# Performance work log

Measured on AMD Instinct MI355X. Metric: run time of the kernel, lower is better.

The kernel has to match this reference:

```python
import jax, jax.numpy as jnp
import numpy as np

EPS = 1e-8  # torch.nn.functional.cosine_similarity default eps


def setup_inputs() -> dict:
    key = jax.random.key(0)
    k1, k2 = jax.random.split(key)
    P, B, D = 64, 512, 1024
    z_list = jax.random.normal(k1, (P, B, D), dtype=jnp.float32)
    z_avg = jax.random.normal(k2, (B, D), dtype=jnp.float32)  # passed but unused (overwritten in forward)
    return {"z_list": z_list, "z_avg": z_avg}


def reference(z_list, z_avg):
    # z_list: (P, B, D). The original overwrites z_avg with the patch mean.
    P, B, _ = z_list.shape
    z_avg = jnp.mean(z_list, axis=0)  # (B, D)

    # cosine_similarity(z_list[p,i], z_avg[j]) via normalize + batched matmul
    zn = z_list / jnp.maximum(jnp.linalg.norm(z_list, axis=-1, keepdims=True), EPS)
    an = z_avg / jnp.maximum(jnp.linalg.norm(z_avg, axis=-1, keepdims=True), EPS)
    cos_sim = jnp.einsum("pbd,cd->pbc", zn, an) - 1.0  # (P, B, B)

    mask = ~jnp.eye(B, dtype=bool)  # zero out diagonal (i == j)
    z_dissim = jnp.sum(cos_sim * mask[None, :, :])
    count = jnp.sum(mask) * P  # B*(B-1)*P
    return z_dissim / count
```

## Files before the change

### kernel.cpp

```cpp
#include <hip/hip_runtime.h>
#include <math.h>

constexpr int P = 64, B = 512, D = 1024;
constexpr int D4 = D / 4;
constexpr int WAVES = 4;
constexpr int PC = P / WAVES;
constexpr int K3B = 32;
constexpr int BPB = B / K3B;
#define EPS 1e-8f

__device__ inline float wave_reduce_sum(float v) {
#pragma unroll
  for (int off = 1; off < 64; off <<= 1) v += __shfl_xor(v, off);
  return v;
}

__device__ inline float dot4(const float4& a, const float4& b) {
  return a.x * b.x + a.y * b.y + a.z * b.z + a.w * b.w;
}

__global__ __launch_bounds__(256) void k_main(const float* __restrict__ z,
                                              float* __restrict__ an,
                                              float* __restrict__ Uv,
                                              float* __restrict__ diag) {
  const int b = blockIdx.x;
  const int t = threadIdx.x;
  const int w = t >> 6;
  const int lane = t & 63;

  __shared__ float4 lds_zs[WAVES][D4];
  __shared__ float4 lds_uu[WAVES][D4];
  __shared__ float red[2 * WAVES];

  float4 zs[4], uu[4];
#pragma unroll
  for (int k = 0; k < 4; ++k) {
    zs[k] = make_float4(0.f, 0.f, 0.f, 0.f);
    uu[k] = make_float4(0.f, 0.f, 0.f, 0.f);
  }

  const size_t pstride = (size_t)B * D4;
  const float4* base = (const float4*)z + ((size_t)(w * PC) * B + b) * D4;

  float4 cur[4];
#pragma unroll
  for (int k = 0; k < 4; ++k) cur[k] = base[k * 64 + lane];

  for (int pp = 0; pp < PC; ++pp) {
    float4 nxt[4];
    if (pp + 1 < PC) {
      const float4* nb = base + (size_t)(pp + 1) * pstride;
#pragma unroll
      for (int k = 0; k < 4; ++k) nxt[k] = nb[k * 64 + lane];
    } else {
#pragma unroll
      for (int k = 0; k < 4; ++k) nxt[k] = cur[k];
    }

    float ss = 0.f;
#pragma unroll
    for (int k = 0; k < 4; ++k) ss += dot4(cur[k], cur[k]);
    ss = wave_reduce_sum(ss);
    const float wgt = 1.0f / fmaxf(sqrtf(ss), EPS);

#pragma unroll
    for (int k = 0; k < 4; ++k) {
      zs[k].x += cur[k].x; zs[k].y += cur[k].y; zs[k].z += cur[k].z; zs[k].w += cur[k].w;
      uu[k].x += wgt * cur[k].x; uu[k].y += wgt * cur[k].y;
      uu[k].z += wgt * cur[k].z; uu[k].w += wgt * cur[k].w;
    }
#pragma unroll
    for (int k = 0; k < 4; ++k) cur[k] = nxt[k];
  }

#pragma unroll
  for (int k = 0; k < 4; ++k) {
    lds_zs[w][k * 64 + lane] = zs[k];
    lds_uu[w][k * 64 + lane] = uu[k];
  }
  __syncthreads();

  float4 zsum = make_float4(0.f, 0.f, 0.f, 0.f);
  float4 usum = make_float4(0.f, 0.f, 0.f, 0.f);
#pragma unroll
  for (int ww = 0; ww < WAVES; ++ww) {
    float4 a = lds_zs[ww][t];
    float4 u = lds_uu[ww][t];
    zsum.x += a.x; zsum.y += a.y; zsum.z += a.z; zsum.w += a.w;
    usum.x += u.x; usum.y += u.y; usum.z += u.z; usum.w += u.w;
  }

  float ss = dot4(zsum, zsum);
  ss = wave_reduce_sum(ss);
  if (lane == 0) red[w] = ss;
  __syncthreads();
  ss = red[0] + red[1] + red[2] + red[3];

  const float inv = 1.0f / fmaxf(sqrtf(ss), (float)P * EPS);
  float4 a4 = make_float4(zsum.x * inv, zsum.y * inv, zsum.z * inv, zsum.w * inv);

  ((float4*)an)[(size_t)b * D4 + t] = a4;
  ((float4*)Uv)[(size_t)b * D4 + t] = usum;

  float dg = dot4(usum, a4);
  dg = wave_reduce_sum(dg);
  if (lane == 0) red[WAVES + w] = dg;
  __syncthreads();
  if (t == 0) diag[b] = red[WAVES] + red[WAVES + 1] + red[WAVES + 2] + red[WAVES + 3];
}

__global__ __launch_bounds__(256) void k3_colsum(const float* __restrict__ an,
                                                 const float* __restrict__ Uv,
                                                 float* __restrict__ Spart,
                                                 float* __restrict__ Tpart) {
  const int blk = blockIdx.x;
  const int t = threadIdx.x;
  float4 s = make_float4(0.f, 0.f, 0.f, 0.f);
  float4 tt = make_float4(0.f, 0.f, 0.f, 0.f);
#pragma unroll 4
  for (int i = 0; i < BPB; ++i) {
    const size_t b = (size_t)blk * BPB + i;
    float4 a = ((const float4*)an)[b * D4 + t];
    float4 u = ((const float4*)Uv)[b * D4 + t];
    s.x += a.x; s.y += a.y; s.z += a.z; s.w += a.w;
    tt.x += u.x; tt.y += u.y; tt.z += u.z; tt.w += u.w;
  }
  ((float4*)Spart)[(size_t)blk * D4 + t] = s;
  ((float4*)Tpart)[(size_t)blk * D4 + t] = tt;
}

__global__ __launch_bounds__(256) void k4_final(const float* __restrict__ Spart,
                                                const float* __restrict__ Tpart,
                                                const float* __restrict__ diag,
                                                float* __restrict__ out) {
  const int t = threadIdx.x;
  __shared__ float red[4];
  float4 S = make_float4(0.f, 0.f, 0.f, 0.f);
  float4 T = make_float4(0.f, 0.f, 0.f, 0.f);
#pragma unroll 4
  for (int blk = 0; blk < K3B; ++blk) {
    float4 s = ((const float4*)Spart)[(size_t)blk * D4 + t];
    float4 u = ((const float4*)Tpart)[(size_t)blk * D4 + t];
    S.x += s.x; S.y += s.y; S.z += s.z; S.w += s.w;
    T.x += u.x; T.y += u.y; T.z += u.z; T.w += u.w;
  }
  float local = dot4(S, T) - diag[t] - diag[t + 256];
  local = wave_reduce_sum(local);
  const int wid = t >> 6;
  if ((t & 63) == 0) red[wid] = local;
  __syncthreads();
  if (t == 0) {
    const float tot = red[0] + red[1] + red[2] + red[3];
    const float count = 64.0f * 512.0f * 511.0f;
    out[0] = tot / count - 1.0f;
  }
}

extern "C" void kernel_launch(void* const* d_in, const int* in_sizes, int n_in,
                              void* d_out, int out_size, void* d_ws, size_t ws_size,
                              hipStream_t stream) {
  const float* z = (const float*)d_in[0];

  float* ws = (float*)d_ws;
  float* an = ws;
  float* Uv = an + (size_t)B * D;
  float* diag = Uv + (size_t)B * D;
  float* Spart = diag + B;
  float* Tpart = Spart + (size_t)K3B * D;

  k_main<<<B, 256, 0, stream>>>(z, an, Uv, diag);
  k3_colsum<<<K3B, 256, 0, stream>>>(an, Uv, Spart, Tpart);
  k4_final<<<1, 256, 0, stream>>>(Spart, Tpart, diag, (float*)d_out);
}
```

Baseline: 36.11 us.

## Double waves per row block and fuse colsum and final into one atomic tail kernel

The main kernel now runs 8 waves per block, each handling fewer patches, to get more memory parallelism, and it zeroes the atomic accumulators from inside the kernel. The separate column-sum and final-reduction kernels become one tail kernel that atomically accumulates S, T and the diagonal sum, then uses a last-block counter to compute the scalar. This removes one launch and the partial-buffer round trip, at the cost of atomic contention and a threadfence-based last-block pattern. The LDS footprint doubles to 64KB per block, which limits occupancy.

```diff
diff --git a/kernel.cpp b/kernel.cpp
--- a/kernel.cpp
+++ b/kernel.cpp
@@ -3,7 +3,7 @@
 
 constexpr int P = 64, B = 512, D = 1024;
 constexpr int D4 = D / 4;
-constexpr int WAVES = 4;
+constexpr int WAVES = 8;
 constexpr int PC = P / WAVES;
 constexpr int K3B = 32;
 constexpr int BPB = B / K3B;
@@ -19,18 +19,24 @@
   return a.x * b.x + a.y * b.y + a.z * b.z + a.w * b.w;
 }
 
-__global__ __launch_bounds__(256) void k_main(const float* __restrict__ z,
-                                              float* __restrict__ an,
-                                              float* __restrict__ Uv,
-                                              float* __restrict__ diag) {
+__global__ __launch_bounds__(512, 4) void k_main(const float* __restrict__ z,
+                                                 float* __restrict__ an,
+                                                 float* __restrict__ Uv,
+                                                 float* __restrict__ diag,
+                                                 float4* __restrict__ zero4) {
   const int b = blockIdx.x;
   const int t = threadIdx.x;
   const int w = t >> 6;
   const int lane = t & 63;
 
+  if (t == 0) {
+    zero4[b] = make_float4(0.f, 0.f, 0.f, 0.f);
+    if (b == 0) zero4[512] = make_float4(0.f, 0.f, 0.f, 0.f);
+  }
+
   __shared__ float4 lds_zs[WAVES][D4];
   __shared__ float4 lds_uu[WAVES][D4];
-  __shared__ float red[2 * WAVES];
+  __shared__ float red[8];
 
   float4 zs[4], uu[4];
 #pragma unroll
@@ -82,39 +88,44 @@
 
   float4 zsum = make_float4(0.f, 0.f, 0.f, 0.f);
   float4 usum = make_float4(0.f, 0.f, 0.f, 0.f);
-#pragma unroll
-  for (int ww = 0; ww < WAVES; ++ww) {
-    float4 a = lds_zs[ww][t];
-    float4 u = lds_uu[ww][t];
-    zsum.x += a.x; zsum.y += a.y; zsum.z += a.z; zsum.w += a.w;
-    usum.x += u.x; usum.y += u.y; usum.z += u.z; usum.w += u.w;
-  }
-
-  float ss = dot4(zsum, zsum);
-  ss = wave_reduce_sum(ss);
-  if (lane == 0) red[w] = ss;
-  __syncthreads();
-  ss = red[0] + red[1] + red[2] + red[3];
-
-  const float inv = 1.0f / fmaxf(sqrtf(ss), (float)P * EPS);
-  float4 a4 = make_float4(zsum.x * inv, zsum.y * inv, zsum.z * inv, zsum.w * inv);
-
-  ((float4*)an)[(size_t)b * D4 + t] = a4;
-  ((float4*)Uv)[(size_t)b * D4 + t] = usum;
-
-  float dg = dot4(usum, a4);
-  dg = wave_reduce_sum(dg);
-  if (lane == 0) red[WAVES + w] = dg;
-  __syncthreads();
-  if (t == 0) diag[b] = red[WAVES] + red[WAVES + 1] + red[WAVES + 2] + red[WAVES + 3];
-}
-
-__global__ __launch_bounds__(256) void k3_colsum(const float* __restrict__ an,
-                                                 const float* __restrict__ Uv,
-                                                 float* __restrict__ Spart,
-                                                 float* __restrict__ Tpart) {
+  if (t < 256) {
+#pragma unroll
+    for (int ww = 0; ww < WAVES; ++ww) {
+      float4 a = lds_zs[ww][t];
+      float4 u = lds_uu[ww][t];
+      zsum.x += a.x; zsum.y += a.y; zsum.z += a.z; zsum.w += a.w;
+      usum.x += u.x; usum.y += u.y; usum.z += u.z; usum.w += u.w;
+    }
+    float ssq = wave_reduce_sum(dot4(zsum, zsum));
+    if (lane == 0) red[w] = ssq;
+  }
+  __syncthreads();
+  if (t < 256) {
+    const float ss2 = red[0] + red[1] + red[2] + red[3];
+    const float inv = 1.0f / fmaxf(sqrtf(ss2), (float)P * EPS);
+    float4 a4 = make_float4(zsum.x * inv, zsum.y * inv, zsum.z * inv, zsum.w * inv);
+
+    ((float4*)an)[(size_t)b * D4 + t] = a4;
+    ((float4*)Uv)[(size_t)b * D4 + t] = usum;
+
+    float dg = wave_reduce_sum(dot4(usum, a4));
+    if (lane == 0) red[4 + w] = dg;
+  }
+  __syncthreads();
+  if (t == 0) diag[b] = red[4] + red[5] + red[6] + red[7];
+}
+
+__global__ __launch_bounds__(256) void k_tail(const float* __restrict__ an,
+                                              const float* __restrict__ Uv,
+                                              const float* __restrict__ diag,
+                                              float* __restrict__ Sfin,
+                                              float* __restrict__ Tfin,
+                                              float* __restrict__ diagsum,
+                                              int* __restrict__ counter,
+                                              float* __restrict__ out) {
   const int blk = blockIdx.x;
   const int t = threadIdx.x;
+
   float4 s = make_float4(0.f, 0.f, 0.f, 0.f);
   float4 tt = make_float4(0.f, 0.f, 0.f, 0.f);
 #pragma unroll 4
@@ -125,34 +136,49 @@
     s.x += a.x; s.y += a.y; s.z += a.z; s.w += a.w;
     tt.x += u.x; tt.y += u.y; tt.z += u.z; tt.w += u.w;
   }
-  ((float4*)Spart)[(size_t)blk * D4 + t] = s;
-  ((float4*)Tpart)[(size_t)blk * D4 + t] = tt;
-}
-
-__global__ __launch_bounds__(256) void k4_final(const float* __restrict__ Spart,
-                                                const float* __restrict__ Tpart,
-                                                const float* __restrict__ diag,
-                                                float* __restrict__ out) {
-  const int t = threadIdx.x;
-  __shared__ float red[4];
-  float4 S = make_float4(0.f, 0.f, 0.f, 0.f);
-  float4 T = make_float4(0.f, 0.f, 0.f, 0.f);
-#pragma unroll 4
-  for (int blk = 0; blk < K3B; ++blk) {
-    float4 s = ((const float4*)Spart)[(size_t)blk * D4 + t];
-    float4 u = ((const float4*)Tpart)[(size_t)blk * D4 + t];
-    S.x += s.x; S.y += s.y; S.z += s.z; S.w += s.w;
-    T.x += u.x; T.y += u.y; T.z += u.z; T.w += u.w;
-  }
-  float local = dot4(S, T) - diag[t] - diag[t + 256];
+  atomicAdd(&Sfin[4 * t + 0], s.x);
+  atomicAdd(&Sfin[4 * t + 1], s.y);
+  atomicAdd(&Sfin[4 * t + 2], s.z);
+  atomicAdd(&Sfin[4 * t + 3], s.w);
+  atomicAdd(&Tfin[4 * t + 0], tt.x);
+  atomicAdd(&Tfin[4 * t + 1], tt.y);
+  atomicAdd(&Tfin[4 * t + 2], tt.z);
+  atomicAdd(&Tfin[4 * t + 3], tt.w);
+
+  if (t < 64) {
+    float dv = (t < BPB) ? diag[blk * BPB + t] : 0.f;
+    dv = wave_reduce_sum(dv);
+    if (t == 0) atomicAdd(diagsum, dv);
+  }
+
+  __threadfence();
+  __syncthreads();
+
+  __shared__ int is_last;
+  if (t == 0) {
+    int old = atomicAdd(counter, 1);
+    is_last = (old == K3B - 1);
+  }
+  __syncthreads();
+  if (!is_last) return;
+
+  __threadfence();
+  float local = 0.f;
+#pragma unroll
+  for (int k = 0; k < 4; ++k) {
+    float sv = __hip_atomic_load(&Sfin[4 * t + k], __ATOMIC_RELAXED, __HIP_MEMORY_SCOPE_AGENT);
+    float tv = __hip_atomic_load(&Tfin[4 * t + k], __ATOMIC_RELAXED, __HIP_MEMORY_SCOPE_AGENT);
+    local += sv * tv;
+  }
   local = wave_reduce_sum(local);
-  const int wid = t >> 6;
-  if ((t & 63) == 0) red[wid] = local;
+  __shared__ float red2[4];
+  if ((t & 63) == 0) red2[t >> 6] = local;
   __syncthreads();
   if (t == 0) {
-    const float tot = red[0] + red[1] + red[2] + red[3];
+    const float dot = red2[0] + red2[1] + red2[2] + red2[3];
+    const float dsum = __hip_atomic_load(diagsum, __ATOMIC_RELAXED, __HIP_MEMORY_SCOPE_AGENT);
     const float count = 64.0f * 512.0f * 511.0f;
-    out[0] = tot / count - 1.0f;
+    out[0] = (dot - dsum) / count - 1.0f;
   }
 }
 
@@ -165,10 +191,13 @@
   float* an = ws;
   float* Uv = an + (size_t)B * D;
   float* diag = Uv + (size_t)B * D;
-  float* Spart = diag + B;
-  float* Tpart = Spart + (size_t)K3B * D;
-
-  k_main<<<B, 256, 0, stream>>>(z, an, Uv, diag);
-  k3_colsum<<<K3B, 256, 0, stream>>>(an, Uv, Spart, Tpart);
-  k4_final<<<1, 256, 0, stream>>>(Spart, Tpart, diag, (float*)d_out);
-}
+  float* Sfin = diag + B;
+  float* Tfin = Sfin + D;
+  float* extras = Tfin + D;
+  float* diagsum = extras;
+  int* counter = (int*)(extras + 1);
+  float4* zero4 = (float4*)Sfin;
+
+  k_main<<<B, 512, 0, stream>>>(z, an, Uv, diag, zero4);
+  k_tail<<<K3B, 256, 0, stream>>>(an, Uv, diag, Sfin, Tfin, diagsum, counter, (float*)d_out);
+}
```

Measured after the change: 41.33 us. +14.5%, slower.
